# Kernel tuning notes

Measured on AMD Instinct MI355X. Metric: run time of the kernel, lower is better.

The kernel has to match this reference:

```python
import jax, jax.numpy as jnp
import numpy as np

B, NH, WH, WW, C, NPOS = 64, 16, 16, 16, 64, 288
N = WH * WW


def setup_inputs() -> dict:
    key = jax.random.key(0)
    k1, k2, k3 = jax.random.split(key, 3)
    query = jax.random.normal(k1, (B, NH, N, C), dtype=jnp.float32)
    attn_logits = jax.random.normal(k2, (B, NH, N, N), dtype=jnp.float32)
    pos_emb = jax.random.normal(k3, (C, NPOS), dtype=jnp.float32) * 0.02
    return {"query": query, "attn_logits": attn_logits, "pos_emb": pos_emb,
            "Wh": WH, "Ww": WW, "npos_max": NPOS}


def _rev_cumsum(x):
    # flip -> cumsum -> flip along last axis
    return jnp.flip(jnp.cumsum(jnp.flip(x, -1), axis=-1), -1)


def reference(query, attn_logits, pos_emb, Wh, Ww, npos_max):
    B_, nH, N_, C_ = query.shape
    gates = jax.nn.sigmoid(attn_logits)                       # (B,nH,N,N)
    gates_h = gates.swapaxes(-1, -2).reshape(B_, nH, N_, Ww, Wh)
    gates_w = gates.reshape(B_, nH, N_, Wh, Ww)
    pos_h = _rev_cumsum(gates_h).reshape(B_, nH, N_, N_).swapaxes(-1, -2)
    pos_w = _rev_cumsum(gates_w).reshape(B_, nH, N_, N_)
    pos = pos_h * Ww + pos_w
    pos = jnp.minimum(pos, npos_max - 1)
    pos_floor = jnp.floor(pos)
    pos_ceil_i = jnp.ceil(pos).astype(jnp.int32)
    pos_floor_i = pos_floor.astype(jnp.int32)
    # (B,nH,N,C) @ (C,npos) -> (B,nH,N,npos)
    logits_int = jnp.einsum('bhnc,cp->bhnp', query, pos_emb)
    logits_ceil = jnp.take_along_axis(logits_int, pos_ceil_i, axis=-1)
    logits_floor = jnp.take_along_axis(logits_int, pos_floor_i, axis=-1)
    w = pos - pos_floor
    return logits_ceil * w + logits_floor * (1.0 - w)
```

## Files before the change

kernel.cpp:

```cpp
#include <hip/hip_runtime.h>


#define NPOS 288
#define NT   18
#define LTS  288

typedef __attribute__((ext_vector_type(8))) short bf16x8;
typedef __attribute__((ext_vector_type(4))) float f32x4;

__device__ __forceinline__ short f2bf(float f) {
    unsigned u = __float_as_uint(f);
    u += 0x7FFF + ((u >> 16) & 1);
    return (short)(u >> 16);
}

template <int D>
__device__ __forceinline__ float suffix_step(float v) {
    int s = __builtin_amdgcn_update_dpp(0, __float_as_int(v), 0x100 | D, 0xF, 0xF, true);
    return v + __int_as_float(s);
}

__global__ void prep_kernel(const float* __restrict__ pos_emb,
                            short* __restrict__ wsb) {
    int idx = blockIdx.x * blockDim.x + threadIdx.x;
    if (idx >= NT * 2 * 64) return;
    int l = idx & 63;
    int s = (idx >> 6) & 1;
    int t = idx >> 7;
    int col = t * 16 + (l & 15);
    int k0  = s * 32 + (l >> 4) * 8;
    short* dst = wsb + idx * 8;
    #pragma unroll
    for (int j = 0; j < 8; ++j)
        dst[j] = f2bf(pos_emb[(k0 + j) * NPOS + col]);
}

__global__ __launch_bounds__(256, 6) void cope2d_kernel(
    const float* __restrict__ query,
    const float* __restrict__ attn_logits,
    const bf16x8* __restrict__ wsb8,
    float* __restrict__ out)
{
    __shared__ float Ltab[16 * LTS];

    const int tid  = threadIdx.x;
    const int lane = tid & 63;
    const int wave = tid >> 6;
    const int blk  = blockIdx.x;
    const int bh   = blk >> 4;
    const int p    = blk & 15;
    const long rowbase = (long)bh * 256 + p * 16;
    const long gbase   = rowbase * 256;

    const float* qptr = query + (rowbase + (lane & 15)) * 64 + (lane >> 4) * 8;
    bf16x8 A[2];
    #pragma unroll
    for (int s = 0; s < 2; ++s) {
        f32x4 lo = *(const f32x4*)(qptr + s * 32);
        f32x4 hi = *(const f32x4*)(qptr + s * 32 + 4);
        #pragma unroll
        for (int j = 0; j < 4; ++j) { A[s][j] = f2bf(lo[j]); A[s][4 + j] = f2bf(hi[j]); }
    }

    float g[16];
    #pragma unroll
    for (int i = 0; i < 16; ++i)
        g[i] = attn_logits[gbase + (long)i * 256 + tid];

    for (int t = wave; t < NT; t += 4) {
        f32x4 c = {0.f, 0.f, 0.f, 0.f};
        c = __builtin_amdgcn_mfma_f32_16x16x32_bf16(A[0], wsb8[(t * 2 + 0) * 64 + lane], c, 0, 0, 0);
        c = __builtin_amdgcn_mfma_f32_16x16x32_bf16(A[1], wsb8[(t * 2 + 1) * 64 + lane], c, 0, 0, 0);
        const int col = t * 16 + (lane & 15);
        const int r0  = (lane >> 4) * 4;
        #pragma unroll
        for (int r = 0; r < 4; ++r)
            Ltab[(r0 + r) * LTS + col] = c[r];
    }
    __syncthreads();

    {
        #pragma unroll
        for (int i = 0; i < 16; ++i)
            g[i] = 1.0f / (1.0f + __expf(-g[i]));

        float sfx[16];
        float run = 0.f;
        #pragma unroll
        for (int i = 15; i >= 0; --i) { run += g[i]; sfx[i] = run; }

        #pragma unroll
        for (int half = 0; half < 2; ++half) {
            const int i0 = half * 8;
            float w8[8]; int fi8[8];
            #pragma unroll
            for (int k = 0; k < 8; ++k) {
                const int i = i0 + k;
                float pw = suffix_step<8>(suffix_step<4>(suffix_step<2>(suffix_step<1>(g[i]))));
                float pos = fminf(sfx[i] * 16.0f + pw, 287.0f);
                float pf = floorf(pos);
                fi8[k] = (int)pf;
                w8[k]  = pos - pf;
            }
            float lf8[8], lc8[8];
            #pragma unroll
            for (int k = 0; k < 8; ++k) {
                const float* Lr = Ltab + (i0 + k) * LTS;
                lf8[k] = Lr[fi8[k]];
                lc8[k] = Lr[fi8[k] + 1];
            }
            #pragma unroll
            for (int k = 0; k < 8; ++k)
                out[gbase + (long)(i0 + k) * 256 + tid] =
                    lf8[k] + w8[k] * (lc8[k] - lf8[k]);
        }
    }
}

extern "C" void kernel_launch(void* const* d_in, const int* in_sizes, int n_in,
                              void* d_out, int out_size, void* d_ws, size_t ws_size,
                              hipStream_t stream) {
    const float* query       = (const float*)d_in[0];
    const float* attn_logits = (const float*)d_in[1];
    const float* pos_emb     = (const float*)d_in[2];
    float* outp = (float*)d_out;
    short* wsb  = (short*)d_ws;

    prep_kernel<<<9, 256, 0, stream>>>(pos_emb, wsb);
    cope2d_kernel<<<16384, 256, 0, stream>>>(query, attn_logits,
                                             (const bf16x8*)d_ws, outp);
}
```

Before: 137.6 us.

## Stage attn_logits via global_load_lds and store logit table in bf16

The attn_logits tile is now streamed straight into LDS with global_load_lds, so the load no longer passes through registers. It is read back from LDS after the barrier. The MFMA B-operand loads are hoisted ahead of the matrix multiplies, and the interpolation table is kept in LDS as bf16 with padded rows. The goal is lower register pressure, more memory-level parallelism and fewer LDS gather costs. The trade-offs are extra rounding from bf16 table values and a larger LDS footprint (about 25KB), which may cut occupancy.

Result: no change. 135.4 us (-1.7%).

```diff
diff --git a/kernel.cpp b/kernel.cpp
--- a/kernel.cpp
+++ b/kernel.cpp
@@ -3,15 +3,18 @@
 
 #define NPOS 288
 #define NT   18
-#define LTS  288
+#define LTS2 292
 
 typedef __attribute__((ext_vector_type(8))) short bf16x8;
 typedef __attribute__((ext_vector_type(4))) float f32x4;
 
-__device__ __forceinline__ short f2bf(float f) {
+__device__ __forceinline__ unsigned short f2bf(float f) {
     unsigned u = __float_as_uint(f);
     u += 0x7FFF + ((u >> 16) & 1);
-    return (short)(u >> 16);
+    return (unsigned short)(u >> 16);
+}
+__device__ __forceinline__ float bf2f(unsigned short b) {
+    return __uint_as_float(((unsigned)b) << 16);
 }
 
 template <int D>
@@ -19,6 +22,10 @@
     int s = __builtin_amdgcn_update_dpp(0, __float_as_int(v), 0x100 | D, 0xF, 0xF, true);
     return v + __int_as_float(s);
 }
+
+#define GLDS(gsrc, ldst) __builtin_amdgcn_global_load_lds(                      \
+    (const __attribute__((address_space(1))) void*)(gsrc),                      \
+    (__attribute__((address_space(3))) void*)(ldst), 16, 0, 0)
 
 __global__ void prep_kernel(const float* __restrict__ pos_emb,
                             short* __restrict__ wsb) {
@@ -32,7 +39,7 @@
     short* dst = wsb + idx * 8;
     #pragma unroll
     for (int j = 0; j < 8; ++j)
-        dst[j] = f2bf(pos_emb[(k0 + j) * NPOS + col]);
+        dst[j] = (short)f2bf(pos_emb[(k0 + j) * NPOS + col]);
 }
 
 __global__ __launch_bounds__(256, 6) void cope2d_kernel(
@@ -41,7 +48,8 @@
     const bf16x8* __restrict__ wsb8,
     float* __restrict__ out)
 {
-    __shared__ float Ltab[16 * LTS];
+    __shared__ float          Gl[16 * 256];
+    __shared__ unsigned short Lb[16 * LTS2];
 
     const int tid  = threadIdx.x;
     const int lane = tid & 63;
@@ -52,6 +60,14 @@
     const long rowbase = (long)bh * 256 + p * 16;
     const long gbase   = rowbase * 256;
 
+    {
+        const float* src = attn_logits + gbase + (long)(wave * 4) * 256 + lane * 4;
+        float* dst = &Gl[(wave * 4) * 256];
+        #pragma unroll
+        for (int r = 0; r < 4; ++r)
+            GLDS(src + r * 256, dst + r * 256);
+    }
+
     const float* qptr = query + (rowbase + (lane & 15)) * 64 + (lane >> 4) * 8;
     bf16x8 A[2];
     #pragma unroll
@@ -59,27 +75,40 @@
         f32x4 lo = *(const f32x4*)(qptr + s * 32);
         f32x4 hi = *(const f32x4*)(qptr + s * 32 + 4);
         #pragma unroll
-        for (int j = 0; j < 4; ++j) { A[s][j] = f2bf(lo[j]); A[s][4 + j] = f2bf(hi[j]); }
+        for (int j = 0; j < 4; ++j) { A[s][j] = (short)f2bf(lo[j]); A[s][4 + j] = (short)f2bf(hi[j]); }
     }
 
-    float g[16];
+    bf16x8 Bf[5][2];
     #pragma unroll
-    for (int i = 0; i < 16; ++i)
-        g[i] = attn_logits[gbase + (long)i * 256 + tid];
+    for (int u = 0; u < 5; ++u) {
+        int t = wave + 4 * u;
+        if (t < NT) {
+            Bf[u][0] = wsb8[(t * 2 + 0) * 64 + lane];
+            Bf[u][1] = wsb8[(t * 2 + 1) * 64 + lane];
+        }
+    }
+    #pragma unroll
+    for (int u = 0; u < 5; ++u) {
+        int t = wave + 4 * u;
+        if (t < NT) {
+            f32x4 c = {0.f, 0.f, 0.f, 0.f};
+            c = __builtin_amdgcn_mfma_f32_16x16x32_bf16(A[0], Bf[u][0], c, 0, 0, 0);
+            c = __builtin_amdgcn_mfma_f32_16x16x32_bf16(A[1], Bf[u][1], c, 0, 0, 0);
+            const int col = t * 16 + (lane & 15);
+            const int r0  = (lane >> 4) * 4;
+            #pragma unroll
+            for (int r = 0; r < 4; ++r)
+                Lb[(r0 + r) * LTS2 + col] = f2bf(c[r]);
+        }
+    }
 
-    for (int t = wave; t < NT; t += 4) {
-        f32x4 c = {0.f, 0.f, 0.f, 0.f};
-        c = __builtin_amdgcn_mfma_f32_16x16x32_bf16(A[0], wsb8[(t * 2 + 0) * 64 + lane], c, 0, 0, 0);
-        c = __builtin_amdgcn_mfma_f32_16x16x32_bf16(A[1], wsb8[(t * 2 + 1) * 64 + lane], c, 0, 0, 0);
-        const int col = t * 16 + (lane & 15);
-        const int r0  = (lane >> 4) * 4;
-        #pragma unroll
-        for (int r = 0; r < 4; ++r)
-            Ltab[(r0 + r) * LTS + col] = c[r];
-    }
     __syncthreads();
 
     {
+        float g[16];
+        #pragma unroll
+        for (int i = 0; i < 16; ++i)
+            g[i] = Gl[i * 256 + tid];
         #pragma unroll
         for (int i = 0; i < 16; ++i)
             g[i] = 1.0f / (1.0f + __expf(-g[i]));
@@ -105,9 +134,9 @@
             float lf8[8], lc8[8];
             #pragma unroll
             for (int k = 0; k < 8; ++k) {
-                const float* Lr = Ltab + (i0 + k) * LTS;
-                lf8[k] = Lr[fi8[k]];
-                lc8[k] = Lr[fi8[k] + 1];
+                const unsigned short* Lr = Lb + (i0 + k) * LTS2;
+                lf8[k] = bf2f(Lr[fi8[k]]);
+                lc8[k] = bf2f(Lr[fi8[k] + 1]);
             }
             #pragma unroll
             for (int k = 0; k < 8; ++k)
```
